# Kernel tuning notes

Hardware: AMD Instinct MI355X
Metric: run time of the kernel (lower is better)

The kernel has to match this reference:

```python
import jax, jax.numpy as jnp
import numpy as np

B, T, H, NH = 2, 2048, 1024, 16
D = H // NH          # head dim = 64
K_CONV = 4           # short conv kernel size


def _dwconv_silu(x, w):
    # causal depthwise conv1d + silu; x:[B,T,C], w:[C,K]
    Kc = w.shape[1]
    xp = jnp.pad(x, ((0, 0), (Kc - 1, 0), (0, 0))).transpose(0, 2, 1)  # [B,C,T+K-1]
    y = jax.lax.conv_general_dilated(xp, w[:, None, :], (1,), 'VALID',
                                     feature_group_count=w.shape[0],
                                     dimension_numbers=('NCH', 'OIH', 'NCH'))
    return jax.nn.silu(y.transpose(0, 2, 1))


def _l2norm(x, eps=1e-6):
    return x * jax.lax.rsqrt(jnp.sum(x * x, -1, keepdims=True) + eps)


def _forward(hidden, Wq, Wk, Wv, conv_q, conv_k, conv_v, Wb, Wa, A_log, dt_bias, Wg, norm_w, Wo):
    Bh, Tt, Hh = hidden.shape
    nh = A_log.shape[0]
    d = Hh // nh
    q = _dwconv_silu(hidden @ Wq.T, conv_q).reshape(Bh, Tt, nh, d)
    k = _dwconv_silu(hidden @ Wk.T, conv_k).reshape(Bh, Tt, nh, d)
    v = _dwconv_silu(hidden @ Wv.T, conv_v).reshape(Bh, Tt, nh, d)
    q = _l2norm(q) * (d ** -0.5)
    k = _l2norm(k)
    beta = jax.nn.sigmoid(hidden @ Wb.T)                                  # [B,T,h]
    g = -jnp.exp(A_log) * jax.nn.softplus(hidden @ Wa.T + dt_bias)        # [B,T,h]

    def step(S, inp):
        qt, kt, vt, gt, bt = inp
        S = S * jnp.exp(gt)[..., None, None]                 # gated decay
        pred = jnp.einsum('bhk,bhkv->bhv', kt, S)            # current memory readout
        dv = (vt - pred) * bt[..., None]                     # delta-rule update
        S = S + jnp.einsum('bhk,bhv->bhkv', kt, dv)
        ot = jnp.einsum('bhk,bhkv->bhv', qt, S)
        return S, ot

    xs = (q.transpose(1, 0, 2, 3), k.transpose(1, 0, 2, 3), v.transpose(1, 0, 2, 3),
          g.transpose(1, 0, 2), beta.transpose(1, 0, 2))
    S0 = jnp.zeros((Bh, nh, d, d), hidden.dtype)
    _, o = jax.lax.scan(step, S0, xs)
    o = o.transpose(1, 0, 2, 3)                               # [B,T,h,d]
    gate = (hidden @ Wg.T).reshape(Bh, Tt, nh, d)
    o = o * jax.lax.rsqrt(jnp.mean(o * o, -1, keepdims=True) + 1e-5) * norm_w
    o = o * jax.nn.silu(gate)                                 # gated RMSNorm
    return o.reshape(Bh, Tt, Hh) @ Wo.T


def setup_inputs():
    key = jax.random.key(0)
    ks = jax.random.split(key, 16)
    s = 0.02
    return {
        'hidden': jax.random.normal(ks[0], (B, T, H), jnp.float32),
        'Wq': jax.random.normal(ks[1], (H, H), jnp.float32) * s,
        'Wk': jax.random.normal(ks[2], (H, H), jnp.float32) * s,
        'Wv': jax.random.normal(ks[3], (H, H), jnp.float32) * s,
        'conv_q': jax.random.normal(ks[4], (H, K_CONV), jnp.float32) * 0.5,
        'conv_k': jax.random.normal(ks[5], (H, K_CONV), jnp.float32) * 0.5,
        'conv_v': jax.random.normal(ks[6], (H, K_CONV), jnp.float32) * 0.5,
        'Wb': jax.random.normal(ks[7], (NH, H), jnp.float32) * s,
        'Wa': jax.random.normal(ks[8], (NH, H), jnp.float32) * s,
        'A_log': jnp.log(jax.random.uniform(ks[9], (NH,), jnp.float32, 1.0, 16.0)),
        'dt_bias': jnp.log(jnp.expm1(jax.random.uniform(ks[10], (NH,), jnp.float32, 1e-3, 0.1))),
        'Wg': jax.random.normal(ks[11], (H, H), jnp.float32) * s,
        'norm_w': jnp.ones((D,), jnp.float32),
        'Wo': jax.random.normal(ks[12], (H, H), jnp.float32) * s,
    }


def reference(hidden, Wq, Wk, Wv, conv_q, conv_k, conv_v, Wb, Wa, A_log, dt_bias, Wg, norm_w, Wo):
    return _forward(hidden, Wq, Wk, Wv, conv_q, conv_k, conv_v, Wb, Wa, A_log, dt_bias, Wg, norm_w, Wo)
```

## Files before the change

kernel.cpp:

```cpp
#include <hip/hip_runtime.h>
#include <hip/hip_bf16.h>

typedef unsigned short u16;
typedef __attribute__((ext_vector_type(4))) float f32x4;
typedef __attribute__((ext_vector_type(8))) short bf16x8;

#define TLEN 2048
#define NHEAD 16
#define HD 1024

__device__ inline u16 f2bf(float f) {
  unsigned x = __float_as_uint(f);
  return (u16)((x + 0x7fffu + ((x >> 16) & 1u)) >> 16);
}
__device__ inline float bf2f(u16 u) { return __uint_as_float(((unsigned)u) << 16); }

__device__ inline unsigned pkbf(float lo, float hi) {
  unsigned r;
  asm("v_cvt_pk_bf16_f32 %0, %1, %2" : "=v"(r) : "v"(lo), "v"(hi));
  return r;
}

__device__ inline void storev(float* p, float v) { *p = v; }
__device__ inline void storev(u16* p, float v)   { *p = f2bf(v); }

__device__ inline int rowx(int row) { return (row ^ (row >> 3)) & 7; }
__device__ inline int swz(int row, int col) {
  return (row << 7) + (((col >> 3) ^ rowx(row)) << 4) + ((col & 7) << 1);
}
__device__ inline bf16x8 frag(const u16* base, int row, int kslot) {
  return *(const bf16x8*)((const char*)base + (row << 7) +
                          ((kslot ^ rowx(row)) << 4));
}

__global__ __launch_bounds__(256) void cvt_all(
    const float* __restrict__ h,  const float* __restrict__ wq,
    const float* __restrict__ wk, const float* __restrict__ wv,
    const float* __restrict__ wg, const float* __restrict__ wo,
    const float* __restrict__ Wb, const float* __restrict__ Wa,
    u16* __restrict__ dh,  u16* __restrict__ dhlo,
    u16* __restrict__ dwq, u16* __restrict__ dwk,
    u16* __restrict__ dwv, u16* __restrict__ dwg, u16* __restrict__ dwo,
    u16* __restrict__ dwba_h, u16* __restrict__ dwba_l) {
  const int b = blockIdx.x;
  if (b < 4096) {
    const size_t i = (size_t)b * 256 + threadIdx.x;
    float4 v = *(const float4*)(h + i * 4);
    ushort4 hi, lo;
    hi.x = f2bf(v.x); lo.x = f2bf(v.x - bf2f(hi.x));
    hi.y = f2bf(v.y); lo.y = f2bf(v.y - bf2f(hi.y));
    hi.z = f2bf(v.z); lo.z = f2bf(v.z - bf2f(hi.z));
    hi.w = f2bf(v.w); lo.w = f2bf(v.w - bf2f(hi.w));
    *(ushort4*)(dh + i * 4) = hi;
    *(ushort4*)(dhlo + i * 4) = lo;
  } else if (b < 9216) {
    const int wsel = (b - 4096) >> 10;
    const size_t i = (size_t)((b - 4096) & 1023) * 256 + threadIdx.x;
    const float* s; u16* d;
    switch (wsel) {
      case 0: s = wq; d = dwq; break;
      case 1: s = wk; d = dwk; break;
      case 2: s = wv; d = dwv; break;
      case 3: s = wg; d = dwg; break;
      default: s = wo; d = dwo; break;
    }
    float4 v = *(const float4*)(s + i * 4);
    ushort4 u;
    u.x = f2bf(v.x); u.y = f2bf(v.y); u.z = f2bf(v.z); u.w = f2bf(v.w);
    *(ushort4*)(d + i * 4) = u;
  } else {
    const size_t i = (size_t)(b - 9216) * 256 + threadIdx.x;
    const size_t flat = i * 4;
    const float* src = (flat < 16384) ? (Wb + flat) : (Wa + (flat - 16384));
    float4 v = *(const float4*)src;
    ushort4 hi, lo;
    hi.x = f2bf(v.x); lo.x = f2bf(v.x - bf2f(hi.x));
    hi.y = f2bf(v.y); lo.y = f2bf(v.y - bf2f(hi.y));
    hi.z = f2bf(v.z); lo.z = f2bf(v.z - bf2f(hi.z));
    hi.w = f2bf(v.w); lo.w = f2bf(v.w - bf2f(hi.w));
    *(ushort4*)(dwba_h + flat) = hi;
    *(ushort4*)(dwba_l + flat) = lo;
  }
}

__global__ __launch_bounds__(256, 2) void gemm_big(
    const u16* __restrict__ A,
    const u16* __restrict__ W0p, const u16* __restrict__ W1p,
    const u16* __restrict__ W2p, const u16* __restrict__ W3p,
    u16* __restrict__ C0, u16* __restrict__ C1,
    u16* __restrict__ C2, u16* __restrict__ C3,
    int M, int N, int K) {
  const u16* W; u16* C;
  switch (blockIdx.z) {
    case 0: W = W0p; C = C0; break;
    case 1: W = W1p; C = C1; break;
    case 2: W = W2p; C = C2; break;
    default: W = W3p; C = C3; break;
  }
  const int tid = threadIdx.x;
  const int lane = tid & 63, wid = tid >> 6;
  const int fr = lane & 15, fq = lane >> 4;
  const int row0 = blockIdx.y * 256, col0 = blockIdx.x * 128;
  __shared__ __align__(16) u16 As[256 * 64];
  __shared__ __align__(16) u16 Bs[128 * 64];

  const u16* aSrc[8]; const u16* bSrc[4];
#pragma unroll
  for (int it = 0; it < 8; ++it) {
    const int s = it * 256 + tid;
    const int r = s >> 3, cc = s & 7;
    aSrc[it] = A + (size_t)(row0 + r) * K + (cc ^ (r & 7)) * 8;
  }
#pragma unroll
  for (int it = 0; it < 4; ++it) {
    const int s = it * 256 + tid;
    const int r = s >> 3, cc = s & 7;
    bSrc[it] = W + (size_t)(col0 + r) * K + (cc ^ (r & 7)) * 8;
  }
  int aOff[4][2], bOff[8][2];
#pragma unroll
  for (int m = 0; m < 4; ++m)
#pragma unroll
    for (int kk = 0; kk < 2; ++kk) {
      const int ra = wid * 64 + m * 16 + fr;
      aOff[m][kk] = ra * 128 + ((((kk << 2) | fq) ^ (ra & 7)) << 4);
    }
#pragma unroll
  for (int n = 0; n < 8; ++n)
#pragma unroll
    for (int kk = 0; kk < 2; ++kk) {
      const int rb = n * 16 + fr;
      bOff[n][kk] = rb * 128 + ((((kk << 2) | fq) ^ (rb & 7)) << 4);
    }

  f32x4 acc[4][8] = {};
  for (int k0 = 0; k0 < K; k0 += 64) {
#pragma unroll
    for (int it = 0; it < 8; ++it)
      __builtin_amdgcn_global_load_lds(
          (const __attribute__((address_space(1))) void*)(aSrc[it] + k0),
          (__attribute__((address_space(3))) void*)((char*)As + (it * 256 + tid) * 16),
          16, 0, 0);
#pragma unroll
    for (int it = 0; it < 4; ++it)
      __builtin_amdgcn_global_load_lds(
          (const __attribute__((address_space(1))) void*)(bSrc[it] + k0),
          (__attribute__((address_space(3))) void*)((char*)Bs + (it * 256 + tid) * 16),
          16, 0, 0);
    __syncthreads();
#pragma unroll
    for (int kk = 0; kk < 2; ++kk) {
      bf16x8 af[4], bfr[8];
#pragma unroll
      for (int m = 0; m < 4; ++m)
        af[m] = *(const bf16x8*)((const char*)As + aOff[m][kk]);
#pragma unroll
      for (int n = 0; n < 8; ++n)
        bfr[n] = *(const bf16x8*)((const char*)Bs + bOff[n][kk]);
#pragma unroll
      for (int m = 0; m < 4; ++m)
#pragma unroll
        for (int n = 0; n < 8; ++n)
          acc[m][n] = __builtin_amdgcn_mfma_f32_16x16x32_bf16(af[m], bfr[n], acc[m][n], 0, 0, 0);
    }
    __syncthreads();
  }
#pragma unroll
  for (int m = 0; m < 4; ++m)
#pragma unroll
    for (int n = 0; n < 8; ++n) {
      const int gr0 = row0 + wid * 64 + m * 16 + fq * 4;
      const int gc = col0 + n * 16 + fr;
      const unsigned c01 = pkbf(acc[m][n][0], acc[m][n][1]);
      const unsigned c23 = pkbf(acc[m][n][2], acc[m][n][3]);
      C[(size_t)(gr0 + 0) * N + gc] = (u16)c01;
      C[(size_t)(gr0 + 1) * N + gc] = (u16)(c01 >> 16);
      C[(size_t)(gr0 + 2) * N + gc] = (u16)c23;
      C[(size_t)(gr0 + 3) * N + gc] = (u16)(c23 >> 16);
    }
}

template <typename OutT, int MT>
__global__ __launch_bounds__(256) void gemm_lin(
    const u16* __restrict__ A, const u16* __restrict__ W,
    OutT* __restrict__ C, int M, int N, int K) {
  const int tid = threadIdx.x;
  const int lane = tid & 63, wid = tid >> 6;
  const int wr = wid >> 1, wc = wid & 1;
  const int fr = lane & 15, fq = lane >> 4;
  const int row0 = blockIdx.y * (MT * 32), col0 = blockIdx.x * 128;
  __shared__ __align__(16) u16 As[MT * 32 * 64];
  __shared__ __align__(16) u16 Bs[128 * 64];

  const u16* aSrc[MT]; const u16* bSrc[4];
#pragma unroll
  for (int it = 0; it < MT; ++it) {
    const int c = it * 256 + tid;
    const int r = c >> 3, cc = c & 7, sc = cc ^ (r & 7);
    aSrc[it] = A + (size_t)(row0 + r) * K + sc * 8;
  }
#pragma unroll
  for (int it = 0; it < 4; ++it) {
    const int c = it * 256 + tid;
    const int r = c >> 3, cc = c & 7, sc = cc ^ (r & 7);
    bSrc[it] = W + (size_t)(col0 + r) * K + sc * 8;
  }
  int aOff[MT][2], bOff[4][2];
#pragma unroll
  for (int m = 0; m < MT; ++m)
#pragma unroll
    for (int kk = 0; kk < 2; ++kk) {
      const int ra = wr * (MT * 16) + m * 16 + fr;
      aOff[m][kk] = ra * 128 + ((((kk << 2) | fq) ^ (fr & 7)) << 4);
    }
#pragma unroll
  for (int n = 0; n < 4; ++n)
#pragma unroll
    for (int kk = 0; kk < 2; ++kk) {
      const int rb = wc * 64 + n * 16 + fr;
      bOff[n][kk] = rb * 128 + ((((kk << 2) | fq) ^ (fr & 7)) << 4);
    }

  f32x4 acc[MT][4] = {};
  for (int k0 = 0; k0 < K; k0 += 64) {
#pragma unroll
    for (int it = 0; it < MT; ++it)
      __builtin_amdgcn_global_load_lds(
          (const __attribute__((address_space(1))) void*)(aSrc[it] + k0),
          (__attribute__((address_space(3))) void*)((char*)As + (it * 256 + wid * 64) * 16),
          16, 0, 0);
#pragma unroll
    for (int it = 0; it < 4; ++it)
      __builtin_amdgcn_global_load_lds(
          (const __attribute__((address_space(1))) void*)(bSrc[it] + k0),
          (__attribute__((address_space(3))) void*)((char*)Bs + (it * 256 + wid * 64) * 16),
          16, 0, 0);
    __syncthreads();
#pragma unroll
    for (int kk = 0; kk < 2; ++kk) {
      bf16x8 af[MT], bfr[4];
#pragma unroll
      for (int m = 0; m < MT; ++m)
        af[m] = *(const bf16x8*)((const char*)As + aOff[m][kk]);
#pragma unroll
      for (int n = 0; n < 4; ++n)
        bfr[n] = *(const bf16x8*)((const char*)Bs + bOff[n][kk]);
#pragma unroll
      for (int m = 0; m < MT; ++m)
#pragma unroll
        for (int n = 0; n < 4; ++n)
          acc[m][n] = __builtin_amdgcn_mfma_f32_16x16x32_bf16(af[m], bfr[n], acc[m][n], 0, 0, 0);
    }
    __syncthreads();
  }
#pragma unroll
  for (int m = 0; m < MT; ++m)
#pragma unroll
    for (int n = 0; n < 4; ++n)
#pragma unroll
      for (int r = 0; r < 4; ++r) {
        const int gr = row0 + wr * (MT * 16) + m * 16 + fq * 4 + r;
        const int gc = col0 + wc * 64 + n * 16 + fr;
        storev(&C[(size_t)gr * N + gc], acc[m][n][r]);
      }
}

__global__ __launch_bounds__(256) void small_mfma(
    const u16* __restrict__ hhi, const u16* __restrict__ hlo,
    const u16* __restrict__ whi, const u16* __restrict__ wlo,
    const float* __restrict__ A_log, const float* __restrict__ dtb,
    float* __restrict__ bbuf, float* __restrict__ gbuf) {
  extern __shared__ char smc[];
  u16* Ahi = (u16*)smc;
  u16* Alo = (u16*)(smc + 32768);
  float* Red = (float*)(smc + 65536);
  const int tid = threadIdx.x;
  const int row0 = blockIdx.x * 16;
#pragma unroll
  for (int i = 0; i < 8; ++i) {
    const int slot = tid + 256 * i;
    const int r = slot >> 7, s = slot & 127;
    const int ss = s ^ (r & 7);
    const size_t src = (size_t)(row0 + r) * 1024 + (size_t)ss * 8;
    __builtin_amdgcn_global_load_lds(
        (const __attribute__((address_space(1))) void*)(hhi + src),
        (__attribute__((address_space(3))) void*)(Ahi + (size_t)slot * 8), 16, 0, 0);
    __builtin_amdgcn_global_load_lds(
        (const __attribute__((address_space(1))) void*)(hlo + src),
        (__attribute__((address_space(3))) void*)(Alo + (size_t)slot * 8), 16, 0, 0);
  }
  __syncthreads();
  const int w = tid >> 6, lane = tid & 63, fr = lane & 15, fq = lane >> 4;
  f32x4 acc[2] = {};
#pragma unroll
  for (int kk = 0; kk < 8; ++kk) {
    const int s = w * 32 + kk * 4 + fq;
    const size_t k = (size_t)w * 256 + kk * 32 + fq * 8;
    const int aoff = ((fr << 7) + (s ^ (fr & 7))) * 8;
    bf16x8 ah = *(const bf16x8*)(Ahi + aoff);
    bf16x8 al = *(const bf16x8*)(Alo + aoff);
#pragma unroll
    for (int ct = 0; ct < 2; ++ct) {
      const size_t boff = (size_t)(ct * 16 + fr) * 1024 + k;
      bf16x8 bh = *(const bf16x8*)(whi + boff);
      bf16x8 bl = *(const bf16x8*)(wlo + boff);
      acc[ct] = __builtin_amdgcn_mfma_f32_16x16x32_bf16(ah, bh, acc[ct], 0, 0, 0);
      acc[ct] = __builtin_amdgcn_mfma_f32_16x16x32_bf16(ah, bl, acc[ct], 0, 0, 0);
      acc[ct] = __builtin_amdgcn_mfma_f32_16x16x32_bf16(al, bh, acc[ct], 0, 0, 0);
    }
  }
#pragma unroll
  for (int ct = 0; ct < 2; ++ct)
#pragma unroll
    for (int rr = 0; rr < 4; ++rr)
      Red[(w * 16 + fq * 4 + rr) * 33 + ct * 16 + fr] = acc[ct][rr];
  __syncthreads();
  if (tid < 128) {
    const int row = tid >> 3, cg = (tid & 7) * 4;
#pragma unroll
    for (int j = 0; j < 4; ++j) {
      const int col = cg + j;
      const float s = Red[(0 * 16 + row) * 33 + col] + Red[(1 * 16 + row) * 33 + col]
                    + Red[(2 * 16 + row) * 33 + col] + Red[(3 * 16 + row) * 33 + col];
      const int grow = row0 + row;
      if (col < 16) {
        bbuf[grow * NHEAD + col] = 1.f / (1.f + __expf(-s));
      } else {
        const int hh = col - 16;
        const float xs = s + dtb[hh];
        const float sp = (xs > 20.f) ? xs : log1pf(__expf(xs));
        gbuf[grow * NHEAD + hh] = -__expf(A_log[hh]) * sp;
      }
    }
  }
}

__global__ __launch_bounds__(512) void chunk_local(
    const u16* __restrict__ qp, const u16* __restrict__ kp, const u16* __restrict__ vp,
    const float* __restrict__ cq, const float* __restrict__ ck, const float* __restrict__ cv,
    const float* __restrict__ gbuf, const float* __restrict__ bbuf,
    u16* __restrict__ Phi, u16* __restrict__ Plo, u16* __restrict__ Ug,
    u16* __restrict__ Rg, u16* __restrict__ Yg) {
  __shared__ __align__(16) u16 Kb[64 * 64];
  __shared__ __align__(16) u16 Qb[64 * 64];
  __shared__ __align__(16) u16 K2T[64 * 64];
  __shared__ __align__(16) u16 KWt[64 * 64];
  __shared__ __align__(16) u16 Vt[64 * 64];
  __shared__ __align__(16) u16 Zb[64 * 64];
  __shared__ __align__(16) u16 Zt[64 * 64];
  __shared__ __align__(16) u16 Mb[64 * 72];
  __shared__ __align__(16) float Cb[16 * 64];
  __shared__ float bcs[64], bet[64], e2v[64], Bv[64];
  u16* WTh = Mb;
  u16* uTh = KWt;
  u16* Gb  = Vt;

  const int bid = blockIdx.x;
  const int c = bid & 31, bh = bid >> 5;
  const int b = bh >> 4, h = bh & 15;
  const int tid = threadIdx.x;

  {
    int* zp = (int*)Zt;
#pragma unroll
    for (int i = 0; i < 4; ++i) zp[tid + 512 * i] = 0;
  }
  if (tid < 64) {
    const size_t gi = (size_t)((b * TLEN + c * 64) + tid) * NHEAD + h;
    bet[tid] = bbuf[gi];
    float v = gbuf[gi];
#pragma unroll
    for (int ofs = 1; ofs < 64; ofs <<= 1) {
      float tt = __shfl_up(v, ofs);
      if (tid >= ofs) v += tt;
    }
    bcs[tid] = v;
  }
  __syncthreads();
  if (tid < 64) {
    const float blast = bcs[63];
    Bv[tid]  = __expf(bcs[tid]);
    e2v[tid] = __expf(blast - bcs[tid]);
  }
  __syncthreads();

  {
    const int dq = (tid & 15) * 4;
    const int col = h * 64 + dq;
    float4 wq4[4], wk4[4], wv4[4];
#pragma unroll
    for (int jj = 0; jj < 4; ++jj) {
      wq4[jj] = *(const float4*)(cq + (size_t)(col + jj) * 4);
      wk4[jj] = *(const float4*)(ck + (size_t)(col + jj) * 4);
      wv4[jj] = *(const float4*)(cv + (size_t)(col + jj) * 4);
    }
#pragma unroll
    for (int i = 0; i < 2; ++i) {
      const int r = i * 32 + (tid >> 4);
      const int tcur = c * 64 + r;
      ushort4 xq[4], xk[4], xv[4];
#pragma unroll
      for (int m = 0; m < 4; ++m) {
        const int tt = tcur - 3 + m;
        if (tt >= 0) {
          const size_t a = (size_t)(b * TLEN + tt) * HD + col;
          xq[m] = *(const ushort4*)(qp + a);
          xk[m] = *(const ushort4*)(kp + a);
          xv[m] = *(const ushort4*)(vp + a);
        } else {
          xq[m] = ushort4{0, 0, 0, 0}; xk[m] = xq[m]; xv[m] = xq[m];
        }
      }
      float yq[4], yk[4], yv[4];
      float ssq = 0.f, ssk = 0.f;
#pragma unroll
      for (int jj = 0; jj < 4; ++jj) {
        float aq = wq4[jj].x * bf2f(((const u16*)&xq[0])[jj]) +
                   wq4[jj].y * bf2f(((const u16*)&xq[1])[jj]) +
                   wq4[jj].z * bf2f(((const u16*)&xq[2])[jj]) +
                   wq4[jj].w * bf2f(((const u16*)&xq[3])[jj]);
        float ak = wk4[jj].x * bf2f(((const u16*)&xk[0])[jj]) +
                   wk4[jj].y * bf2f(((const u16*)&xk[1])[jj]) +
                   wk4[jj].z * bf2f(((const u16*)&xk[2])[jj]) +
                   wk4[jj].w * bf2f(((const u16*)&xk[3])[jj]);
        float av = wv4[jj].x * bf2f(((const u16*)&xv[0])[jj]) +
                   wv4[jj].y * bf2f(((const u16*)&xv[1])[jj]) +
                   wv4[jj].z * bf2f(((const u16*)&xv[2])[jj]) +
                   wv4[jj].w * bf2f(((const u16*)&xv[3])[jj]);
        yq[jj] = aq / (1.f + __expf(-aq));
        yk[jj] = ak / (1.f + __expf(-ak));
        yv[jj] = av / (1.f + __expf(-av));
        ssq += yq[jj] * yq[jj];
        ssk += yk[jj] * yk[jj];
      }
      ssq += __shfl_xor(ssq, 1); ssq += __shfl_xor(ssq, 2);
      ssq += __shfl_xor(ssq, 4); ssq += __shfl_xor(ssq, 8);
      ssk += __shfl_xor(ssk, 1); ssk += __shfl_xor(ssk, 2);
      ssk += __shfl_xor(ssk, 4); ssk += __shfl_xor(ssk, 8);
      const float qsc = rsqrtf(ssq + 1e-6f) * 0.125f;
      const float ksc = rsqrtf(ssk + 1e-6f);
      const float bR = bet[r], e2R = e2v[r], wscR = bR * Bv[r];
      float kvf[4];
#pragma unroll
      for (int jj = 0; jj < 4; ++jj) kvf[jj] = yk[jj] * ksc;
      uint2 qo2, ko2;
      qo2.x = pkbf(yq[0] * qsc, yq[1] * qsc);
      qo2.y = pkbf(yq[2] * qsc, yq[3] * qsc);
      ko2.x = pkbf(kvf[0], kvf[1]);
      ko2.y = pkbf(kvf[2], kvf[3]);
      *(uint2*)((char*)Qb + swz(r, dq)) = qo2;
      *(uint2*)((char*)Kb + swz(r, dq)) = ko2;
      const unsigned k2a = pkbf(kvf[0] * e2R, kvf[1] * e2R);
      const unsigned k2b = pkbf(kvf[2] * e2R, kvf[3] * e2R);
      const unsigned kwa = pkbf(kvf[0] * wscR, kvf[1] * wscR);
      const unsigned kwb = pkbf(kvf[2] * wscR, kvf[3] * wscR);
      const unsigned vta = pkbf(yv[0] * bR, yv[1] * bR);
      const unsigned vtb = pkbf(yv[2] * bR, yv[3] * bR);
      *(u16*)((char*)K2T + swz(dq + 0, r)) = (u16)k2a;
      *(u16*)((char*)K2T + swz(dq + 1, r)) = (u16)(k2a >> 16);
      *(u16*)((char*)K2T + swz(dq + 2, r)) = (u16)k2b;
      *(u16*)((char*)K2T + swz(dq + 3, r)) = (u16)(k2b >> 16);
      *(u16*)((char*)KWt + swz(dq + 0, r)) = (u16)kwa;
      *(u16*)((char*)KWt + swz(dq + 1, r)) = (u16)(kwa >> 16);
      *(u16*)((char*)KWt + swz(dq + 2, r)) = (u16)kwb;
      *(u16*)((char*)KWt + swz(dq + 3, r)) = (u16)(kwb >> 16);
      *(u16*)((char*)Vt + swz(dq + 0, r)) = (u16)vta;
      *(u16*)((char*)Vt + swz(dq + 1, r)) = (u16)(vta >> 16);
      *(u16*)((char*)Vt + swz(dq + 2, r)) = (u16)vtb;
      *(u16*)((char*)Vt + swz(dq + 3, r)) = (u16)(vtb >> 16);
    }
  }
  __syncthreads();

  const int w = tid >> 6, lane = tid & 63, fr = lane & 15, fq = lane >> 4;
  const int wr = w >> 1;
  const int tc0 = (w & 1) * 2;
  const int t0r = wr * 16 + fq * 4;
  {
    bf16x8 ka0 = frag(Kb, wr * 16 + fr, fq);
    bf16x8 ka1 = frag(Kb, wr * 16 + fr, 4 + fq);
#pragma unroll
    for (int j = 0; j < 2; ++j) {
      const int tc = tc0 + j;
      bf16x8 kb0 = frag(Kb, tc * 16 + fr, fq);
      bf16x8 kb1 = frag(Kb, tc * 16 + fr, 4 + fq);
      f32x4 a = {};
      a = __builtin_amdgcn_mfma_f32_16x16x32_bf16(ka0, kb0, a, 0, 0, 0);
      a = __builtin_amdgcn_mfma_f32_16x16x32_bf16(ka1, kb1, a, 0, 0, 0);
      const int s = tc * 16 + fr;
      float mv[4];
#pragma unroll
      for (int rr = 0; rr < 4; ++rr) {
        const int t = t0r + rr;
        mv[rr] = (s < t) ? bet[t] * __expf(bcs[t] - bcs[s]) * a[rr] : 0.f;
      }
      const unsigned m01 = pkbf(mv[0], mv[1]), m23 = pkbf(mv[2], mv[3]);
      Mb[(t0r + 0) * 72 + s] = (u16)m01;
      Mb[(t0r + 1) * 72 + s] = (u16)(m01 >> 16);
      Mb[(t0r + 2) * 72 + s] = (u16)m23;
      Mb[(t0r + 3) * 72 + s] = (u16)(m23 >> 16);
    }
  }
  __syncthreads();

#pragma unroll 1
  for (int bi = 0; bi < 4; ++bi) {
    if (w < 4) {
      const char* mrow = (const char*)Mb + (size_t)(bi * 16 + fr) * 144;
      bf16x8 ma0 = *(const bf16x8*)(mrow + fq * 16);
      bf16x8 ma1 = *(const bf16x8*)(mrow + 64 + fq * 16);
      bf16x8 zt0 = frag(Zt, w * 16 + fr, fq);
      bf16x8 zt1 = frag(Zt, w * 16 + fr, 4 + fq);
      f32x4 a = {};
      a = __builtin_amdgcn_mfma_f32_16x16x32_bf16(ma0, zt0, a, 0, 0, 0);
      a = __builtin_amdgcn_mfma_f32_16x16x32_bf16(ma1, zt1, a, 0, 0, 0);
#pragma unroll
      for (int rr = 0; rr < 4; ++rr)
        Cb[(fq * 4 + rr) * 64 + w * 16 + fr] = a[rr];
    }
    __syncthreads();
    if (tid < 64) {
      const int j = tid;
      float z[16];
#pragma unroll
      for (int t = 0; t < 16; ++t) {
        float acc = ((bi * 16 + t) == j ? 1.f : 0.f) - Cb[t * 64 + j];
        const u16* mrow = Mb + (size_t)(bi * 16 + t) * 72 + bi * 16;
#pragma unroll
        for (int s = 0; s < t; ++s) acc -= bf2f(mrow[s]) * z[s];
        z[t] = acc;
      }
      unsigned zw[8];
#pragma unroll
      for (int t2 = 0; t2 < 8; ++t2) zw[t2] = pkbf(z[2 * t2], z[2 * t2 + 1]);
#pragma unroll
      for (int t2 = 0; t2 < 8; ++t2) {
        *(u16*)((char*)Zb + swz(bi * 16 + 2 * t2, j)) = (u16)zw[t2];
        *(u16*)((char*)Zb + swz(bi * 16 + 2 * t2 + 1, j)) = (u16)(zw[t2] >> 16);
      }
#pragma unroll
      for (int t4 = 0; t4 < 4; ++t4) {
        uint2 zz; zz.x = zw[2 * t4]; zz.y = zw[2 * t4 + 1];
        *(uint2*)((char*)Zt + swz(j, bi * 16 + t4 * 4)) = zz;
      }
    }
    __syncthreads();
  }

  f32x4 accW[2], accu[2], accG[2];
  {
    bf16x8 kw0 = frag(KWt, wr * 16 + fr, fq), kw1 = frag(KWt, wr * 16 + fr, 4 + fq);
    bf16x8 vt0 = frag(Vt,  wr * 16 + fr, fq), vt1 = frag(Vt,  wr * 16 + fr, 4 + fq);
    bf16x8 qa0 = frag(Qb,  wr * 16 + fr, fq), qa1 = frag(Qb,  wr * 16 + fr, 4 + fq);
#pragma unroll
    for (int j = 0; j < 2; ++j) {
      const int tc = tc0 + j;
      bf16x8 z0 = frag(Zb, tc * 16 + fr, fq), z1 = frag(Zb, tc * 16 + fr, 4 + fq);
      bf16x8 kb0 = frag(Kb, tc * 16 + fr, fq), kb1 = frag(Kb, tc * 16 + fr, 4 + fq);
      f32x4 aw = {}, au = {}, ag = {};
      aw = __builtin_amdgcn_mfma_f32_16x16x32_bf16(kw0, z0, aw, 0, 0, 0);
      aw = __builtin_amdgcn_mfma_f32_16x16x32_bf16(kw1, z1, aw, 0, 0, 0);
      au = __builtin_amdgcn_mfma_f32_16x16x32_bf16(vt0, z0, au, 0, 0, 0);
      au = __builtin_amdgcn_mfma_f32_16x16x32_bf16(vt1, z1, au, 0, 0, 0);
      ag = __builtin_amdgcn_mfma_f32_16x16x32_bf16(qa0, kb0, ag, 0, 0, 0);
      ag = __builtin_amdgcn_mfma_f32_16x16x32_bf16(qa1, kb1, ag, 0, 0, 0);
      accW[j] = aw; accu[j] = au; accG[j] = ag;
    }
  }
  __syncthreads();
#pragma unroll
  for (int j = 0; j < 2; ++j) {
    const int tc = tc0 + j;
    const int co = tc * 16 + fr;
    const unsigned w01 = pkbf(accW[j][0], accW[j][1]);
    const unsigned w23 = pkbf(accW[j][2], accW[j][3]);
    const unsigned u01 = pkbf(accu[j][0], accu[j][1]);
    const unsigned u23 = pkbf(accu[j][2], accu[j][3]);
    float gv[4];
#pragma unroll
    for (int rr = 0; rr < 4; ++rr) {
      const int ro = t0r + rr;
      gv[rr] = (co <= ro) ? accG[j][rr] * __expf(bcs[ro] - bcs[co]) : 0.f;
    }
    const unsigned g01 = pkbf(gv[0], gv[1]), g23 = pkbf(gv[2], gv[3]);
    *(u16*)((char*)WTh + swz(t0r + 0, co)) = (u16)w01;
    *(u16*)((char*)WTh + swz(t0r + 1, co)) = (u16)(w01 >> 16);
    *(u16*)((char*)WTh + swz(t0r + 2, co)) = (u16)w23;
    *(u16*)((char*)WTh + swz(t0r + 3, co)) = (u16)(w23 >> 16);
    *(u16*)((char*)uTh + swz(t0r + 0, co)) = (u16)u01;
    *(u16*)((char*)uTh + swz(t0r + 1, co)) = (u16)(u01 >> 16);
    *(u16*)((char*)uTh + swz(t0r + 2, co)) = (u16)u23;
    *(u16*)((char*)uTh + swz(t0r + 3, co)) = (u16)(u23 >> 16);
    *(u16*)((char*)Gb + swz(t0r + 0, co)) = (u16)g01;
    *(u16*)((char*)Gb + swz(t0r + 1, co)) = (u16)(g01 >> 16);
    *(u16*)((char*)Gb + swz(t0r + 2, co)) = (u16)g23;
    *(u16*)((char*)Gb + swz(t0r + 3, co)) = (u16)(g23 >> 16);
  }
  __syncthreads();

  {
    bf16x8 k20 = frag(K2T, wr * 16 + fr, fq), k21 = frag(K2T, wr * 16 + fr, 4 + fq);
    bf16x8 g0  = frag(Gb,  wr * 16 + fr, fq), g1  = frag(Gb,  wr * 16 + fr, 4 + fq);
    const float bl = Bv[63];
    const size_t off = (size_t)bid * 4096;
#pragma unroll
    for (int j = 0; j < 2; ++j) {
      const int tc = tc0 + j;
      bf16x8 w0 = frag(WTh, tc * 16 + fr, fq), w1 = frag(WTh, tc * 16 + fr, 4 + fq);
      bf16x8 u0 = frag(uTh, tc * 16 + fr, fq), u1 = frag(uTh, tc * 16 + fr, 4 + fq);
      f32x4 aP = {}, aU = {}, aR = {}, aY = {};
      aP = __builtin_amdgcn_mfma_f32_16x16x32_bf16(k20, w0, aP, 0, 0, 0);
      aP = __builtin_amdgcn_mfma_f32_16x16x32_bf16(k21, w1, aP, 0, 0, 0);
      aU = __builtin_amdgcn_mfma_f32_16x16x32_bf16(k20, u0, aU, 0, 0, 0);
      aU = __builtin_amdgcn_mfma_f32_16x16x32_bf16(k21, u1, aU, 0, 0, 0);
      aR = __builtin_amdgcn_mfma_f32_16x16x32_bf16(g0, w0, aR, 0, 0, 0);
      aR = __builtin_amdgcn_mfma_f32_16x16x32_bf16(g1, w1, aR, 0, 0, 0);
      aY = __builtin_amdgcn_mfma_f32_16x16x32_bf16(g0, u0, aY, 0, 0, 0);
      aY = __builtin_amdgcn_mfma_f32_16x16x32_bf16(g1, u1, aY, 0, 0, 0);
      const int cb = tc * 16 + fr;
      float pv[4], rv[4];
#pragma unroll
      for (int rr = 0; rr < 4; ++rr) {
        const int ar = t0r + rr;
        pv[rr] = ((ar == cb) ? bl : 0.f) - aP[rr];
        const float qv = bf2f(*(const u16*)((const char*)Qb + swz(ar, cb)));
        rv[rr] = Bv[ar] * qv - aR[rr];
      }
      const unsigned p01 = pkbf(pv[0], pv[1]), p23 = pkbf(pv[2], pv[3]);
      const float l0 = pv[0] - bf2f((u16)p01), l1 = pv[1] - bf2f((u16)(p01 >> 16));
      const float l2 = pv[2] - bf2f((u16)p23), l3 = pv[3] - bf2f((u16)(p23 >> 16));
      const unsigned q01 = pkbf(l0, l1), q23 = pkbf(l2, l3);
      const unsigned u01 = pkbf(aU[0], aU[1]), u23 = pkbf(aU[2], aU[3]);
      const unsigned r01 = pkbf(rv[0], rv[1]), r23 = pkbf(rv[2], rv[3]);
      const unsigned y01 = pkbf(aY[0], aY[1]), y23 = pkbf(aY[2], aY[3]);
      const size_t o0 = off + (size_t)(t0r + 0) * 64 + cb;
      const size_t o1 = off + (size_t)(t0r + 1) * 64 + cb;
      const size_t o2 = off + (size_t)(t0r + 2) * 64 + cb;
      const size_t o3 = off + (size_t)(t0r + 3) * 64 + cb;
      Phi[o0] = (u16)p01; Phi[o1] = (u16)(p01 >> 16);
      Phi[o2] = (u16)p23; Phi[o3] = (u16)(p23 >> 16);
      Plo[o0] = (u16)q01; Plo[o1] = (u16)(q01 >> 16);
      Plo[o2] = (u16)q23; Plo[o3] = (u16)(q23 >> 16);
      Ug[o0] = (u16)u01; Ug[o1] = (u16)(u01 >> 16);
      Ug[o2] = (u16)u23; Ug[o3] = (u16)(u23 >> 16);
      Rg[o0] = (u16)r01; Rg[o1] = (u16)(r01 >> 16);
      Rg[o2] = (u16)r23; Rg[o3] = (u16)(r23 >> 16);
      Yg[o0] = (u16)y01; Yg[o1] = (u16)(y01 >> 16);
      Yg[o2] = (u16)y23; Yg[o3] = (u16)(y23 >> 16);
    }
  }
}

__global__ __launch_bounds__(256) void state_step(
    const u16* __restrict__ Phi, const u16* __restrict__ Plo,
    const u16* __restrict__ Ug, u16* __restrict__ Sst) {
  __shared__ __align__(16) u16 Sth[2][64 * 64];
  __shared__ __align__(16) u16 Stl[2][64 * 64];
  const int bh = blockIdx.x;
  const int tid = threadIdx.x;
  const int w = tid >> 6, lane = tid & 63, fr = lane & 15, fq = lane >> 4;
  const int ar0 = w * 16 + fq * 4;
  const size_t bbase = (size_t)bh * 32 * 4096;
  {
    int* p0 = (int*)&Sth[0][0];
    int* p1 = (int*)&Stl[0][0];
#pragma unroll
    for (int i = 0; i < 8; ++i) { p0[tid + 256 * i] = 0; p1[tid + 256 * i] = 0; }
    const ushort4 z4 = {0, 0, 0, 0};
#pragma unroll
    for (int i = 0; i < 4; ++i)
      *(ushort4*)(Sst + bbase + (size_t)tid * 16 + i * 4) = z4;
  }
  bf16x8 ph[2], pl[2];
  float uin[4][4];
#pragma unroll
  for (int kk = 0; kk < 2; ++kk) {
    const size_t ao = bbase + (size_t)(w * 16 + fr) * 64 + (kk * 4 + fq) * 8;
    ph[kk] = *(const bf16x8*)(Phi + ao);
    pl[kk] = *(const bf16x8*)(Plo + ao);
  }
#pragma unroll
  for (int tc = 0; tc < 4; ++tc)
#pragma unroll
    for (int rr = 0; rr < 4; ++rr)
      uin[tc][rr] = bf2f(Ug[bbase + (size_t)(ar0 + rr) * 64 + tc * 16 + fr]);
  __syncthreads();
  int cur = 0;
  for (int c = 0; c < 32; ++c) {
    f32x4 acc[4];
    bf16x8 phc[2] = {ph[0], ph[1]}, plc[2] = {pl[0], pl[1]};
#pragma unroll
    for (int tc = 0; tc < 4; ++tc)
#pragma unroll
      for (int rr = 0; rr < 4; ++rr) acc[tc][rr] = uin[tc][rr];
    if (c + 1 < 32) {
      const size_t off = bbase + (size_t)(c + 1) * 4096;
#pragma unroll
      for (int kk = 0; kk < 2; ++kk) {
        const size_t ao = off + (size_t)(w * 16 + fr) * 64 + (kk * 4 + fq) * 8;
        ph[kk] = *(const bf16x8*)(Phi + ao);
        pl[kk] = *(const bf16x8*)(Plo + ao);
      }
#pragma unroll
      for (int tc = 0; tc < 4; ++tc)
#pragma unroll
        for (int rr = 0; rr < 4; ++rr)
          uin[tc][rr] = bf2f(Ug[off + (size_t)(ar0 + rr) * 64 + tc * 16 + fr]);
    }
#pragma unroll
    for (int tc = 0; tc < 4; ++tc) {
#pragma unroll
      for (int kk = 0; kk < 2; ++kk) {
        bf16x8 sh = frag(&Sth[cur][0], tc * 16 + fr, kk * 4 + fq);
        bf16x8 sl = frag(&Stl[cur][0], tc * 16 + fr, kk * 4 + fq);
        acc[tc] = __builtin_amdgcn_mfma_f32_16x16x32_bf16(phc[kk], sh, acc[tc], 0, 0, 0);
        acc[tc] = __builtin_amdgcn_mfma_f32_16x16x32_bf16(phc[kk], sl, acc[tc], 0, 0, 0);
        acc[tc] = __builtin_amdgcn_mfma_f32_16x16x32_bf16(plc[kk], sh, acc[tc], 0, 0, 0);
      }
    }
    const int nxt = cur ^ 1;
    const size_t offn = bbase + (size_t)(c + 1) * 4096;
#pragma unroll
    for (int tc = 0; tc < 4; ++tc) {
      const int col = tc * 16 + fr;
      const unsigned h01 = pkbf(acc[tc][0], acc[tc][1]);
      const unsigned h23 = pkbf(acc[tc][2], acc[tc][3]);
      const float l0 = acc[tc][0] - bf2f((u16)h01);
      const float l1 = acc[tc][1] - bf2f((u16)(h01 >> 16));
      const float l2 = acc[tc][2] - bf2f((u16)h23);
      const float l3 = acc[tc][3] - bf2f((u16)(h23 >> 16));
      uint2 hh; hh.x = h01; hh.y = h23;
      uint2 ll; ll.x = pkbf(l0, l1); ll.y = pkbf(l2, l3);
      *(uint2*)((char*)&Sth[nxt][0] + swz(col, ar0)) = hh;
      *(uint2*)((char*)&Stl[nxt][0] + swz(col, ar0)) = ll;
      if (c + 1 < 32)
        *(uint2*)(Sst + offn + (size_t)col * 64 + ar0) = hh;
    }
    cur = nxt;
    __syncthreads();
  }
}

__global__ __launch_bounds__(256) void chunk_out(
    const u16* __restrict__ Rg, const u16* __restrict__ Yg,
    const u16* __restrict__ SstT, const u16* __restrict__ gatep,
    const float* __restrict__ norm_w, u16* __restrict__ outb) {
  const int bid = blockIdx.x;
  const int c = bid & 31, bh = bid >> 5, b = bh >> 4, h = bh & 15;
  const int tid = threadIdx.x;
  const int w = tid >> 6, lane = tid & 63, fr = lane & 15, fq = lane >> 4;
  const int ar0 = w * 16 + fq * 4;
  const size_t off = (size_t)bid * 4096;
  bf16x8 ra[2];
#pragma unroll
  for (int kk = 0; kk < 2; ++kk)
    ra[kk] = *(const bf16x8*)(Rg + off + (size_t)(w * 16 + fr) * 64 + (kk * 4 + fq) * 8);
  f32x4 acc[4];
#pragma unroll
  for (int tc = 0; tc < 4; ++tc)
#pragma unroll
    for (int rr = 0; rr < 4; ++rr)
      acc[tc][rr] = bf2f(Yg[off + (size_t)(ar0 + rr) * 64 + tc * 16 + fr]);
#pragma unroll
  for (int tc = 0; tc < 4; ++tc)
#pragma unroll
    for (int kk = 0; kk < 2; ++kk) {
      bf16x8 sb = *(const bf16x8*)(SstT + off + (size_t)(tc * 16 + fr) * 64 + (kk * 4 + fq) * 8);
      acc[tc] = __builtin_amdgcn_mfma_f32_16x16x32_bf16(ra[kk], sb, acc[tc], 0, 0, 0);
    }
  float nwv[4];
#pragma unroll
  for (int tc = 0; tc < 4; ++tc) nwv[tc] = norm_w[tc * 16 + fr];
  const size_t btbase = (size_t)(b * TLEN + c * 64);
#pragma unroll
  for (int rr = 0; rr < 4; ++rr) {
    const int t = ar0 + rr;
    float rs = acc[0][rr] * acc[0][rr] + acc[1][rr] * acc[1][rr]
             + acc[2][rr] * acc[2][rr] + acc[3][rr] * acc[3][rr];
    rs += __shfl_xor(rs, 1); rs += __shfl_xor(rs, 2);
    rs += __shfl_xor(rs, 4); rs += __shfl_xor(rs, 8);
    const float inv = rsqrtf(rs * (1.0f / 64.0f) + 1e-5f);
    const size_t rowoff = (btbase + t) * 1024 + h * 64;
#pragma unroll
    for (int tc = 0; tc < 4; ++tc) {
      const int j = tc * 16 + fr;
      const float g = bf2f(gatep[rowoff + j]);
      const float val = acc[tc][rr] * inv * nwv[tc] * (g / (1.f + __expf(-g)));
      outb[rowoff + j] = f2bf(val);
    }
  }
}

extern "C" void kernel_launch(void* const* d_in, const int* in_sizes, int n_in,
                              void* d_out, int out_size, void* d_ws, size_t ws_size,
                              hipStream_t stream) {
  const float* hidden = (const float*)d_in[0];
  const float* Wq     = (const float*)d_in[1];
  const float* Wk     = (const float*)d_in[2];
  const float* Wv     = (const float*)d_in[3];
  const float* cq     = (const float*)d_in[4];
  const float* ck     = (const float*)d_in[5];
  const float* cv     = (const float*)d_in[6];
  const float* Wb     = (const float*)d_in[7];
  const float* Wa     = (const float*)d_in[8];
  const float* A_log  = (const float*)d_in[9];
  const float* dtb    = (const float*)d_in[10];
  const float* Wg     = (const float*)d_in[11];
  const float* nw     = (const float*)d_in[12];
  const float* Wo     = (const float*)d_in[13];

  char* p = (char*)d_ws;
  const size_t MB = 1u << 20;
  u16* h_bf = (u16*)(p + 0 * MB);
  u16* wq_b = (u16*)(p + 8 * MB);
  u16* wk_b = (u16*)(p + 10 * MB);
  u16* wv_b = (u16*)(p + 12 * MB);
  u16* wg_b = (u16*)(p + 14 * MB);
  u16* Phi = (u16*)(p + 0 * MB);
  u16* Plo = (u16*)(p + 8 * MB);
  u16* wo_b = (u16*)(p + 16 * MB);
  u16* qp_b = (u16*)(p + 18 * MB);
  u16* kp_b = (u16*)(p + 26 * MB);
  u16* vp_b = (u16*)(p + 34 * MB);
  u16* gp_b = (u16*)(p + 42 * MB);
  u16*   of_b = vp_b;
  float* gbuf = (float*)(p + 50 * MB);
  float* bbuf = (float*)(p + 50 * MB + 262144);
  u16* Ug  = (u16*)(p + 51 * MB);
  u16* Rg  = (u16*)(p + 59 * MB);
  u16* Yg  = (u16*)(p + 67 * MB);
  u16* Sst = (u16*)(p + 75 * MB);
  u16* hlo_b = (u16*)(p + 83 * MB);
  u16* wba_h = (u16*)(p + 91 * MB);
  u16* wba_l = (u16*)(p + 91 * MB + 65536);

  cvt_all<<<9248, 256, 0, stream>>>(hidden, Wq, Wk, Wv, Wg, Wo, Wb, Wa,
                                    h_bf, hlo_b, wq_b, wk_b, wv_b, wg_b, wo_b,
                                    wba_h, wba_l);

  gemm_big<<<dim3(8, 16, 4), 256, 0, stream>>>(
      h_bf, wq_b, wk_b, wv_b, wg_b, qp_b, kp_b, vp_b, gp_b, 4096, 1024, 1024);

  const int sm_lds = 65536 + 8448;
  hipFuncSetAttribute((const void*)small_mfma,
                      hipFuncAttributeMaxDynamicSharedMemorySize, sm_lds);
  small_mfma<<<256, 256, sm_lds, stream>>>(h_bf, hlo_b, wba_h, wba_l,
                                           A_log, dtb, bbuf, gbuf);

  chunk_local<<<1024, 512, 0, stream>>>(qp_b, kp_b, vp_b, cq, ck, cv,
                                        gbuf, bbuf, Phi, Plo, Ug, Rg, Yg);
  state_step<<<32, 256, 0, stream>>>(Phi, Plo, Ug, Sst);
  chunk_out<<<1024, 256, 0, stream>>>(Rg, Yg, Sst, gp_b, nw, of_b);

  gemm_lin<float, 2><<<dim3(8, 64, 1), 256, 0, stream>>>(
      of_b, wo_b, (float*)d_out, 4096, 1024, 1024);
}
```

Baseline: 168.4 us.

## Split state recurrence across column groups and reuse big GEMM for output projection

The sequential chunk-state kernel is split so that each block handles 16 of the 64 state columns, giving four times as many blocks (128 instead of 32). Column groups are independent in the recurrence, so this shortens the serial critical path per block. Separately, the output projection drops the smaller-tile gemm_lin and uses the templated 256x128-tile gemm_big with a float store path. The larger tile cuts the grid to 128 blocks, which may underfill the GPU.

```diff
diff --git a/kernel.cpp b/kernel.cpp
--- a/kernel.cpp
+++ b/kernel.cpp
@@ -20,9 +20,6 @@
   asm("v_cvt_pk_bf16_f32 %0, %1, %2" : "=v"(r) : "v"(lo), "v"(hi));
   return r;
 }
-
-__device__ inline void storev(float* p, float v) { *p = v; }
-__device__ inline void storev(u16* p, float v)   { *p = f2bf(v); }
 
 __device__ inline int rowx(int row) { return (row ^ (row >> 3)) & 7; }
 __device__ inline int swz(int row, int col) {
@@ -83,14 +80,15 @@
   }
 }
 
+template <typename OutT>
 __global__ __launch_bounds__(256, 2) void gemm_big(
     const u16* __restrict__ A,
     const u16* __restrict__ W0p, const u16* __restrict__ W1p,
     const u16* __restrict__ W2p, const u16* __restrict__ W3p,
-    u16* __restrict__ C0, u16* __restrict__ C1,
-    u16* __restrict__ C2, u16* __restrict__ C3,
+    OutT* __restrict__ C0, OutT* __restrict__ C1,
+    OutT* __restrict__ C2, OutT* __restrict__ C3,
     int M, int N, int K) {
-  const u16* W; u16* C;
+  const u16* W; OutT* C;
   switch (blockIdx.z) {
     case 0: W = W0p; C = C0; break;
     case 1: W = W1p; C = C1; break;
@@ -171,98 +169,19 @@
     for (int n = 0; n < 8; ++n) {
       const int gr0 = row0 + wid * 64 + m * 16 + fq * 4;
       const int gc = col0 + n * 16 + fr;
-      const unsigned c01 = pkbf(acc[m][n][0], acc[m][n][1]);
-      const unsigned c23 = pkbf(acc[m][n][2], acc[m][n][3]);
-      C[(size_t)(gr0 + 0) * N + gc] = (u16)c01;
-      C[(size_t)(gr0 + 1) * N + gc] = (u16)(c01 >> 16);
-      C[(size_t)(gr0 + 2) * N + gc] = (u16)c23;
-      C[(size_t)(gr0 + 3) * N + gc] = (u16)(c23 >> 16);
-    }
-}
-
-template <typename OutT, int MT>
-__global__ __launch_bounds__(256) void gemm_lin(
-    const u16* __restrict__ A, const u16* __restrict__ W,
-    OutT* __restrict__ C, int M, int N, int K) {
-  const int tid = threadIdx.x;
-  const int lane = tid & 63, wid = tid >> 6;
-  const int wr = wid >> 1, wc = wid & 1;
-  const int fr = lane & 15, fq = lane >> 4;
-  const int row0 = blockIdx.y * (MT * 32), col0 = blockIdx.x * 128;
-  __shared__ __align__(16) u16 As[MT * 32 * 64];
-  __shared__ __align__(16) u16 Bs[128 * 64];
-
-  const u16* aSrc[MT]; const u16* bSrc[4];
-#pragma unroll
-  for (int it = 0; it < MT; ++it) {
-    const int c = it * 256 + tid;
-    const int r = c >> 3, cc = c & 7, sc = cc ^ (r & 7);
-    aSrc[it] = A + (size_t)(row0 + r) * K + sc * 8;
-  }
-#pragma unroll
-  for (int it = 0; it < 4; ++it) {
-    const int c = it * 256 + tid;
-    const int r = c >> 3, cc = c & 7, sc = cc ^ (r & 7);
-    bSrc[it] = W + (size_t)(col0 + r) * K + sc * 8;
-  }
-  int aOff[MT][2], bOff[4][2];
-#pragma unroll
-  for (int m = 0; m < MT; ++m)
-#pragma unroll
-    for (int kk = 0; kk < 2; ++kk) {
-      const int ra = wr * (MT * 16) + m * 16 + fr;
-      aOff[m][kk] = ra * 128 + ((((kk << 2) | fq) ^ (fr & 7)) << 4);
-    }
-#pragma unroll
-  for (int n = 0; n < 4; ++n)
-#pragma unroll
-    for (int kk = 0; kk < 2; ++kk) {
-      const int rb = wc * 64 + n * 16 + fr;
-      bOff[n][kk] = rb * 128 + ((((kk << 2) | fq) ^ (fr & 7)) << 4);
-    }
-
-  f32x4 acc[MT][4] = {};
-  for (int k0 = 0; k0 < K; k0 += 64) {
-#pragma unroll
-    for (int it = 0; it < MT; ++it)
-      __builtin_amdgcn_global_load_lds(
-          (const __attribute__((address_space(1))) void*)(aSrc[it] + k0),
-          (__attribute__((address_space(3))) void*)((char*)As + (it * 256 + wid * 64) * 16),
-          16, 0, 0);
-#pragma unroll
-    for (int it = 0; it < 4; ++it)
-      __builtin_amdgcn_global_load_lds(
-          (const __attribute__((address_space(1))) void*)(bSrc[it] + k0),
-          (__attribute__((address_space(3))) void*)((char*)Bs + (it * 256 + wid * 64) * 16),
-          16, 0, 0);
-    __syncthreads();
-#pragma unroll
-    for (int kk = 0; kk < 2; ++kk) {
-      bf16x8 af[MT], bfr[4];
-#pragma unroll
-      for (int m = 0; m < MT; ++m)
-        af[m] = *(const bf16x8*)((const char*)As + aOff[m][kk]);
-#pragma unroll
-      for (int n = 0; n < 4; ++n)
-        bfr[n] = *(const bf16x8*)((const char*)Bs + bOff[n][kk]);
-#pragma unroll
-      for (int m = 0; m < MT; ++m)
-#pragma unroll
-        for (int n = 0; n < 4; ++n)
-          acc[m][n] = __builtin_amdgcn_mfma_f32_16x16x32_bf16(af[m], bfr[n], acc[m][n], 0, 0, 0);
-    }
-    __syncthreads();
-  }
-#pragma unroll
-  for (int m = 0; m < MT; ++m)
-#pragma unroll
-    for (int n = 0; n < 4; ++n)
-#pragma unroll
-      for (int r = 0; r < 4; ++r) {
-        const int gr = row0 + wr * (MT * 16) + m * 16 + fq * 4 + r;
-        const int gc = col0 + wc * 64 + n * 16 + fr;
-        storev(&C[(size_t)gr * N + gc], acc[m][n][r]);
-      }
+      if constexpr (sizeof(OutT) == 2) {
+        const unsigned c01 = pkbf(acc[m][n][0], acc[m][n][1]);
+        const unsigned c23 = pkbf(acc[m][n][2], acc[m][n][3]);
+        C[(size_t)(gr0 + 0) * N + gc] = (OutT)(u16)c01;
+        C[(size_t)(gr0 + 1) * N + gc] = (OutT)(u16)(c01 >> 16);
+        C[(size_t)(gr0 + 2) * N + gc] = (OutT)(u16)c23;
+        C[(size_t)(gr0 + 3) * N + gc] = (OutT)(u16)(c23 >> 16);
+      } else {
+#pragma unroll
+        for (int r = 0; r < 4; ++r)
+          C[(size_t)(gr0 + r) * N + gc] = acc[m][n][r];
+      }
+    }
 }
 
 __global__ __launch_bounds__(256) void small_mfma(
@@ -654,9 +573,11 @@
 __global__ __launch_bounds__(256) void state_step(
     const u16* __restrict__ Phi, const u16* __restrict__ Plo,
     const u16* __restrict__ Ug, u16* __restrict__ Sst) {
-  __shared__ __align__(16) u16 Sth[2][64 * 64];
-  __shared__ __align__(16) u16 Stl[2][64 * 64];
-  const int bh = blockIdx.x;
+  __shared__ __align__(16) u16 Sth[2][16 * 64];
+  __shared__ __align__(16) u16 Stl[2][16 * 64];
+  const int bid = blockIdx.x;
+  const int bh = bid & 31, jg = bid >> 5;
+  const int j0 = jg * 16;
   const int tid = threadIdx.x;
   const int w = tid >> 6, lane = tid & 63, fr = lane & 15, fq = lane >> 4;
   const int ar0 = w * 16 + fq * 4;
@@ -665,14 +586,13 @@
     int* p0 = (int*)&Sth[0][0];
     int* p1 = (int*)&Stl[0][0];
 #pragma unroll
-    for (int i = 0; i < 8; ++i) { p0[tid + 256 * i] = 0; p1[tid + 256 * i] = 0; }
+    for (int i = 0; i < 2; ++i) { p0[tid + 256 * i] = 0; p1[tid + 256 * i] = 0; }
     const ushort4 z4 = {0, 0, 0, 0};
-#pragma unroll
-    for (int i = 0; i < 4; ++i)
-      *(ushort4*)(Sst + bbase + (size_t)tid * 16 + i * 4) = z4;
+    const int e = tid * 4;
+    *(ushort4*)(Sst + bbase + (size_t)(j0 + (e >> 6)) * 64 + (e & 63)) = z4;
   }
   bf16x8 ph[2], pl[2];
-  float uin[4][4];
+  float uin[4];
 #pragma unroll
   for (int kk = 0; kk < 2; ++kk) {
     const size_t ao = bbase + (size_t)(w * 16 + fr) * 64 + (kk * 4 + fq) * 8;
@@ -680,19 +600,15 @@
     pl[kk] = *(const bf16x8*)(Plo + ao);
   }
 #pragma unroll
-  for (int tc = 0; tc < 4; ++tc)
-#pragma unroll
-    for (int rr = 0; rr < 4; ++rr)
-      uin[tc][rr] = bf2f(Ug[bbase + (size_t)(ar0 + rr) * 64 + tc * 16 + fr]);
+  for (int rr = 0; rr < 4; ++rr)
+    uin[rr] = bf2f(Ug[bbase + (size_t)(ar0 + rr) * 64 + j0 + fr]);
   __syncthreads();
   int cur = 0;
   for (int c = 0; c < 32; ++c) {
-    f32x4 acc[4];
+    f32x4 acc;
     bf16x8 phc[2] = {ph[0], ph[1]}, plc[2] = {pl[0], pl[1]};
 #pragma unroll
-    for (int tc = 0; tc < 4; ++tc)
-#pragma unroll
-      for (int rr = 0; rr < 4; ++rr) acc[tc][rr] = uin[tc][rr];
+    for (int rr = 0; rr < 4; ++rr) acc[rr] = uin[rr];
     if (c + 1 < 32) {
       const size_t off = bbase + (size_t)(c + 1) * 4096;
 #pragma unroll
@@ -702,39 +618,32 @@
         pl[kk] = *(const bf16x8*)(Plo + ao);
       }
 #pragma unroll
-      for (int tc = 0; tc < 4; ++tc)
-#pragma unroll
-        for (int rr = 0; rr < 4; ++rr)
-          uin[tc][rr] = bf2f(Ug[off + (size_t)(ar0 + rr) * 64 + tc * 16 + fr]);
-    }
-#pragma unroll
-    for (int tc = 0; tc < 4; ++tc) {
-#pragma unroll
-      for (int kk = 0; kk < 2; ++kk) {
-        bf16x8 sh = frag(&Sth[cur][0], tc * 16 + fr, kk * 4 + fq);
-        bf16x8 sl = frag(&Stl[cur][0], tc * 16 + fr, kk * 4 + fq);
-        acc[tc] = __builtin_amdgcn_mfma_f32_16x16x32_bf16(phc[kk], sh, acc[tc], 0, 0, 0);
-        acc[tc] = __builtin_amdgcn_mfma_f32_16x16x32_bf16(phc[kk], sl, acc[tc], 0, 0, 0);
-        acc[tc] = __builtin_amdgcn_mfma_f32_16x16x32_bf16(plc[kk], sh, acc[tc], 0, 0, 0);
-      }
+      for (int rr = 0; rr < 4; ++rr)
+        uin[rr] = bf2f(Ug[off + (size_t)(ar0 + rr) * 64 + j0 + fr]);
+    }
+#pragma unroll
+    for (int kk = 0; kk < 2; ++kk) {
+      bf16x8 sh = frag(&Sth[cur][0], fr, kk * 4 + fq);
+      bf16x8 sl = frag(&Stl[cur][0], fr, kk * 4 + fq);
+      acc = __builtin_amdgcn_mfma_f32_16x16x32_bf16(phc[kk], sh, acc, 0, 0, 0);
+      acc = __builtin_amdgcn_mfma_f32_16x16x32_bf16(phc[kk], sl, acc, 0, 0, 0);
+      acc = __builtin_amdgcn_mfma_f32_16x16x32_bf16(plc[kk], sh, acc, 0, 0, 0);
     }
     const int nxt = cur ^ 1;
     const size_t offn = bbase + (size_t)(c + 1) * 4096;
-#pragma unroll
-    for (int tc = 0; tc < 4; ++tc) {
-      const int col = tc * 16 + fr;
-      const unsigned h01 = pkbf(acc[tc][0], acc[tc][1]);
-      const unsigned h23 = pkbf(acc[tc][2], acc[tc][3]);
-      const float l0 = acc[tc][0] - bf2f((u16)h01);
-      const float l1 = acc[tc][1] - bf2f((u16)(h01 >> 16));
-      const float l2 = acc[tc][2] - bf2f((u16)h23);
-      const float l3 = acc[tc][3] - bf2f((u16)(h23 >> 16));
+    {
+      const unsigned h01 = pkbf(acc[0], acc[1]);
+      const unsigned h23 = pkbf(acc[2], acc[3]);
+      const float l0 = acc[0] - bf2f((u16)h01);
+      const float l1 = acc[1] - bf2f((u16)(h01 >> 16));
+      const float l2 = acc[2] - bf2f((u16)h23);
+      const float l3 = acc[3] - bf2f((u16)(h23 >> 16));
       uint2 hh; hh.x = h01; hh.y = h23;
       uint2 ll; ll.x = pkbf(l0, l1); ll.y = pkbf(l2, l3);
-      *(uint2*)((char*)&Sth[nxt][0] + swz(col, ar0)) = hh;
-      *(uint2*)((char*)&Stl[nxt][0] + swz(col, ar0)) = ll;
+      *(uint2*)((char*)&Sth[nxt][0] + swz(fr, ar0)) = hh;
+      *(uint2*)((char*)&Stl[nxt][0] + swz(fr, ar0)) = ll;
       if (c + 1 < 32)
-        *(uint2*)(Sst + offn + (size_t)col * 64 + ar0) = hh;
+        *(uint2*)(Sst + offn + (size_t)(j0 + fr) * 64 + ar0) = hh;
     }
     cur = nxt;
     __syncthreads();
@@ -838,7 +747,7 @@
                                     h_bf, hlo_b, wq_b, wk_b, wv_b, wg_b, wo_b,
                                     wba_h, wba_l);
 
-  gemm_big<<<dim3(8, 16, 4), 256, 0, stream>>>(
+  gemm_big<u16><<<dim3(8, 16, 4), 256, 0, stream>>>(
       h_bf, wq_b, wk_b, wv_b, wg_b, qp_b, kp_b, vp_b, gp_b, 4096, 1024, 1024);
 
   const int sm_lds = 65536 + 8448;
@@ -849,9 +758,11 @@
 
   chunk_local<<<1024, 512, 0, stream>>>(qp_b, kp_b, vp_b, cq, ck, cv,
                                         gbuf, bbuf, Phi, Plo, Ug, Rg, Yg);
-  state_step<<<32, 256, 0, stream>>>(Phi, Plo, Ug, Sst);
+  state_step<<<128, 256, 0, stream>>>(Phi, Plo, Ug, Sst);
   chunk_out<<<1024, 256, 0, stream>>>(Rg, Yg, Sst, gp_b, nw, of_b);
 
-  gemm_lin<float, 2><<<dim3(8, 64, 1), 256, 0, stream>>>(
-      of_b, wo_b, (float*)d_out, 4096, 1024, 1024);
-}
+  gemm_big<float><<<dim3(8, 16, 1), 256, 0, stream>>>(
+      of_b, wo_b, wo_b, wo_b, wo_b,
+      (float*)d_out, (float*)d_out, (float*)d_out, (float*)d_out,
+      4096, 1024, 1024);
+}
```

After: 164.7 us, median of 2. 1.02x faster.
